# Kernel tuning notes

Hardware: AMD Instinct MI355X
Metric: run time of the kernel (lower is better)

Reference implementation:

```python
import jax, jax.numpy as jnp
import numpy as np

MARGIN = 1.0  # init kwarg 'margin'
N, D = 8192, 128
NUM_CLASSES = 100

def setup_inputs() -> dict:
    key = jax.random.key(0)
    kx, ky = jax.random.split(key)
    x = jax.random.normal(kx, (N, D), dtype=jnp.float32)
    y = jax.random.randint(ky, (N,), 0, NUM_CLASSES, dtype=jnp.int64)
    return {"x": x, "y": y}

def reference(x, y):
    # Squared euclidean pairwise distances: d[i,j] = sum_k (x[i,k] - x[j,k])^2
    # computed via the ||a||^2 + ||b||^2 - 2 a.b expansion to avoid an NxNxD
    # intermediate. Clamp tiny negatives from fp roundoff.
    sq = jnp.sum(x * x, axis=-1)                      # [N]
    d = sq[:, None] + sq[None, :] - 2.0 * (x @ x.T)   # [N, N]
    d = jnp.maximum(d, 0.0)
    same = (y[:, None] == y[None, :]).astype(x.dtype)  # [N, N] positive-pair mask
    # Faithful to the torch module: dissimilar pairs contribute d, similar
    # pairs contribute hinge clamp(margin - d, 0); mean over all N*N pairs.
    loss = jnp.mean((1.0 - same) * d + same * jnp.maximum(MARGIN - d, 0.0))
    return loss
```

## Files before the change

kernel.cpp:

```cpp
#include <hip/hip_runtime.h>


#define N_ROWS 8192
#define DIM    128
#define NCLS   100
#define CAP    224
#define SCB    1024
#define GBPC   8
#define GRAMB  (NCLS * GBPC)
#define NREP   8

typedef _Float16 half8  __attribute__((ext_vector_type(8)));
typedef _Float16 half4v __attribute__((ext_vector_type(4)));
typedef float    float4v __attribute__((ext_vector_type(4)));

__global__ __launch_bounds__(256) void scan_kernel(
    const float* __restrict__ x, const int* __restrict__ y,
    int* __restrict__ cnt, int* __restrict__ idx,
    _Float16* __restrict__ ghrow, float* __restrict__ sqn,
    float* __restrict__ Scol8, float* __restrict__ SQc8)
{
    const int b = blockIdx.x, tid = threadIdx.x;
    const int l = tid & 31, g = tid >> 5;
    const int r = b * 8 + g;
    const int rep = b & (NREP - 1);
    const float4* x4 = (const float4*)x;
    __shared__ float4 colred[256];

    float4 v = x4[r * 32 + l];
    half4v h;
    h[0] = (_Float16)v.x; h[1] = (_Float16)v.y;
    h[2] = (_Float16)v.z; h[3] = (_Float16)v.w;
    *(half4v*)(ghrow + (size_t)r * DIM + l * 4) = h;

    float s = v.x*v.x + v.y*v.y + v.z*v.z + v.w*v.w;
    s += __shfl_xor(s, 1);  s += __shfl_xor(s, 2);  s += __shfl_xor(s, 4);
    s += __shfl_xor(s, 8);  s += __shfl_xor(s, 16);
    const int c = y[r];
    if (l == 0) {
        sqn[r] = s;
        atomicAdd(&SQc8[rep * NCLS + c], s);
        const int p = atomicAdd(&cnt[c], 1);
        if (p < CAP) idx[c * CAP + p] = r;
    }

    colred[tid] = v;
    __syncthreads();
    if (tid < 32) {
        float4 a = colred[tid];
        #pragma unroll
        for (int gg = 1; gg < 8; ++gg) {
            float4 t = colred[tid + 32 * gg];
            a.x += t.x; a.y += t.y; a.z += t.z; a.w += t.w;
        }
        float* dst = Scol8 + rep * DIM;
        atomicAdd(&dst[4 * tid + 0], a.x);
        atomicAdd(&dst[4 * tid + 1], a.y);
        atomicAdd(&dst[4 * tid + 2], a.z);
        atomicAdd(&dst[4 * tid + 3], a.w);
    }
}

__global__ __launch_bounds__(256) void gram_kernel(
    const _Float16* __restrict__ ghrow, const float* __restrict__ sqn,
    const int* __restrict__ idx, const int* __restrict__ cnt,
    const float* __restrict__ Scol8, const float* __restrict__ SQc8,
    float* __restrict__ Hsum, float* __restrict__ SSsum,
    int* __restrict__ done, float* __restrict__ out)
{
    const int c = blockIdx.x >> 3, qq = blockIdx.x & 7, tid = threadIdx.x;
    __shared__ float wred[8];
    __shared__ int   lastFlag;

    const int mtrue = cnt[c];
    const int m = mtrue < CAP ? mtrue : CAP;
    const int ntiles = (m + 15) >> 4;
    const int ntp = ntiles * (ntiles + 1) / 2;

    const int wave = tid >> 6, lane = tid & 63;
    const int lr = lane & 15, q = lane >> 4;
    float hacc = 0.f, dsum = 0.f;
    const int cbase = c * CAP;

    for (int tp = qq * 4 + wave; tp < ntp; tp += 32) {
        int ta = 0, rem = tp;
        while (rem >= ntiles - ta) { rem -= ntiles - ta; ++ta; }
        const int tb = ta + rem;
        const int raI = ta * 16 + lr, rbI = tb * 16 + lr;
        const int rowA = idx[cbase + (raI < m ? raI : m - 1)];
        const int rowB = idx[cbase + (rbI < m ? rbI : m - 1)];
        const half8* ap = (const half8*)(ghrow + (size_t)rowA * DIM + q * 8);
        const half8* bp = (const half8*)(ghrow + (size_t)rowB * DIM + q * 8);
        float4v acc = {0.f, 0.f, 0.f, 0.f};
        #pragma unroll
        for (int kb = 0; kb < 4; ++kb)
            acc = __builtin_amdgcn_mfma_f32_16x16x32_f16(ap[kb * 4], bp[kb * 4], acc, 0, 0, 0);
        const float w = (ta == tb) ? 1.f : 2.f;
        const int bb = rbI;
        const float sqb = (bb < m) ? sqn[rowB] : 0.f;
        const float sqa_own = sqn[rowA];
        #pragma unroll
        for (int i = 0; i < 4; ++i) {
            const int a = ta * 16 + q * 4 + i;
            const float sqa = __shfl(sqa_own, q * 4 + i, 16);
            if (a < m && bb < m) {
                const float dot = acc[i];
                dsum += w * dot;
                if (a != bb) {
                    float d = fmaxf(sqa + sqb - 2.f * dot, 0.f);
                    hacc += w * fmaxf(1.f - d, 0.f);
                }
            }
        }
    }
    #pragma unroll
    for (int off = 32; off > 0; off >>= 1) {
        hacc += __shfl_xor(hacc, off);
        dsum += __shfl_xor(dsum, off);
    }
    if (lane == 0) { wred[wave] = hacc; wred[4 + wave] = dsum; }
    __syncthreads();
    if (tid == 0) {
        float h = wred[0] + wred[1] + wred[2] + wred[3];
        float d = wred[4] + wred[5] + wred[6] + wred[7];
        if (h != 0.f) atomicAdd(Hsum, h);
        if (d != 0.f) atomicAdd(SSsum, d);
        __threadfence();
        int p = atomicAdd(done, 1);
        lastFlag = (p == GRAMB - 1);
    }
    __syncthreads();
    if (!lastFlag) return;

    __threadfence();
    const double Nf = (double)N_ROWS;
    double contrib = 0.0;
    if (tid < DIM) {
        float sc = 0.f;
        #pragma unroll
        for (int k = 0; k < NREP; ++k) sc += Scol8[k * DIM + tid];
        contrib -= 2.0 * (double)sc * (double)sc;
    }
    if (tid < NCLS) {
        float qv = 0.f;
        #pragma unroll
        for (int k = 0; k < NREP; ++k) qv += SQc8[k * NCLS + tid];
        contrib += 2.0 * (double)qv * (Nf - (double)cnt[tid]);
    }
    if (tid == 0) {
        float H  = __hip_atomic_load(Hsum,  __ATOMIC_RELAXED, __HIP_MEMORY_SCOPE_AGENT);
        float SS = __hip_atomic_load(SSsum, __ATOMIC_RELAXED, __HIP_MEMORY_SCOPE_AGENT);
        contrib += 2.0 * (double)SS + (double)H + Nf * 1.0 ;
    }
    __shared__ double dred[256];
    dred[tid] = contrib;
    __syncthreads();
    for (int s = 128; s > 0; s >>= 1) {
        if (tid < s) dred[tid] += dred[tid + s];
        __syncthreads();
    }
    if (tid == 0) out[0] = (float)(dred[0] / (Nf * Nf));
}

extern "C" void kernel_launch(void* const* d_in, const int* in_sizes, int n_in,
                              void* d_out, int out_size, void* d_ws, size_t ws_size,
                              hipStream_t stream) {
    const float* x = (const float*)d_in[0];
    const int*   y = (const int*)d_in[1];

    _Float16* ghrow = (_Float16*)d_ws;
    float* sqn   = (float*)(ghrow + (size_t)N_ROWS * DIM);
    int*   idx   = (int*)(sqn + N_ROWS);
    float* Scol8 = (float*)(idx + NCLS * CAP);
    float* SQc8  = Scol8 + NREP * DIM;
    float* Hsum  = SQc8 + NREP * NCLS;
    float* SSsum = Hsum + 1;
    int*   cnt   = (int*)(SSsum + 1);
    int*   done  = cnt + NCLS;
    const size_t zero_words = NREP * DIM + NREP * NCLS + 2 + NCLS + 1;

    hipMemsetAsync(Scol8, 0, zero_words * sizeof(float), stream);
    scan_kernel<<<SCB,   256, 0, stream>>>(x, y, cnt, idx, ghrow, sqn,
                                           Scol8, SQc8);
    gram_kernel<<<GRAMB, 256, 0, stream>>>(ghrow, sqn, idx, cnt, Scol8, SQc8,
                                           Hsum, SSsum, done, (float*)d_out);
}
```

Measured before the change: 115.1 us.

## Build per-class row lists in-block via ballot scan instead of global atomics

```diff
diff --git a/kernel.cpp b/kernel.cpp
--- a/kernel.cpp
+++ b/kernel.cpp
@@ -15,10 +15,9 @@
 typedef float    float4v __attribute__((ext_vector_type(4)));
 
 __global__ __launch_bounds__(256) void scan_kernel(
-    const float* __restrict__ x, const int* __restrict__ y,
-    int* __restrict__ cnt, int* __restrict__ idx,
+    const float* __restrict__ x,
     _Float16* __restrict__ ghrow, float* __restrict__ sqn,
-    float* __restrict__ Scol8, float* __restrict__ SQc8)
+    float* __restrict__ Scol8)
 {
     const int b = blockIdx.x, tid = threadIdx.x;
     const int l = tid & 31, g = tid >> 5;
@@ -36,13 +35,7 @@
     float s = v.x*v.x + v.y*v.y + v.z*v.z + v.w*v.w;
     s += __shfl_xor(s, 1);  s += __shfl_xor(s, 2);  s += __shfl_xor(s, 4);
     s += __shfl_xor(s, 8);  s += __shfl_xor(s, 16);
-    const int c = y[r];
-    if (l == 0) {
-        sqn[r] = s;
-        atomicAdd(&SQc8[rep * NCLS + c], s);
-        const int p = atomicAdd(&cnt[c], 1);
-        if (p < CAP) idx[c * CAP + p] = r;
-    }
+    if (l == 0) sqn[r] = s;
 
     colred[tid] = v;
     __syncthreads();
@@ -63,32 +56,60 @@
 
 __global__ __launch_bounds__(256) void gram_kernel(
     const _Float16* __restrict__ ghrow, const float* __restrict__ sqn,
-    const int* __restrict__ idx, const int* __restrict__ cnt,
-    const float* __restrict__ Scol8, const float* __restrict__ SQc8,
+    const int* __restrict__ y,
+    const float* __restrict__ Scol8,
     float* __restrict__ Hsum, float* __restrict__ SSsum,
+    double* __restrict__ Dterm,
     int* __restrict__ done, float* __restrict__ out)
 {
     const int c = blockIdx.x >> 3, qq = blockIdx.x & 7, tid = threadIdx.x;
-    __shared__ float wred[8];
+    __shared__ int   lidx[CAP];
+    __shared__ int   lmv[2];
+    __shared__ float wred[12];
     __shared__ int   lastFlag;
 
-    const int mtrue = cnt[c];
-    const int m = mtrue < CAP ? mtrue : CAP;
+    if (tid < 64) {
+        int base = 0;
+        const int4* y4 = (const int4*)y;
+        int4 vv = y4[tid];
+        for (int it = 0; it < N_ROWS / 256; ++it) {
+            const int4 cur = vv;
+            if (it < N_ROWS / 256 - 1) vv = y4[(it + 1) * 64 + tid];
+            const int rbase = (it * 64 + tid) * 4;
+            #pragma unroll
+            for (int j = 0; j < 4; ++j) {
+                const int yi = (j == 0) ? cur.x : (j == 1) ? cur.y
+                             : (j == 2) ? cur.z : cur.w;
+                const unsigned long long mb = __ballot(yi == c);
+                if (yi == c) {
+                    const int pos = base +
+                        (int)__popcll(mb & ((1ull << tid) - 1ull));
+                    if (pos < CAP) lidx[pos] = rbase + j;
+                }
+                base += (int)__popcll(mb);
+            }
+        }
+        if (tid == 0) { lmv[1] = base; lmv[0] = base < CAP ? base : CAP; }
+    }
+    __syncthreads();
+    const int m = lmv[0], mt = lmv[1];
+
     const int ntiles = (m + 15) >> 4;
     const int ntp = ntiles * (ntiles + 1) / 2;
 
     const int wave = tid >> 6, lane = tid & 63;
     const int lr = lane & 15, q = lane >> 4;
     float hacc = 0.f, dsum = 0.f;
-    const int cbase = c * CAP;
+
+    float qv = (qq == 0 && tid < m) ? sqn[lidx[tid]] : 0.f;
 
     for (int tp = qq * 4 + wave; tp < ntp; tp += 32) {
         int ta = 0, rem = tp;
         while (rem >= ntiles - ta) { rem -= ntiles - ta; ++ta; }
         const int tb = ta + rem;
         const int raI = ta * 16 + lr, rbI = tb * 16 + lr;
-        const int rowA = idx[cbase + (raI < m ? raI : m - 1)];
-        const int rowB = idx[cbase + (rbI < m ? rbI : m - 1)];
+        const int rowA = lidx[raI < m ? raI : m - 1];
+        const int rowB = lidx[rbI < m ? rbI : m - 1];
         const half8* ap = (const half8*)(ghrow + (size_t)rowA * DIM + q * 8);
         const half8* bp = (const half8*)(ghrow + (size_t)rowB * DIM + q * 8);
         float4v acc = {0.f, 0.f, 0.f, 0.f};
@@ -117,12 +138,17 @@
     for (int off = 32; off > 0; off >>= 1) {
         hacc += __shfl_xor(hacc, off);
         dsum += __shfl_xor(dsum, off);
-    }
-    if (lane == 0) { wred[wave] = hacc; wred[4 + wave] = dsum; }
+        qv   += __shfl_xor(qv,   off);
+    }
+    if (lane == 0) { wred[wave] = hacc; wred[4 + wave] = dsum; wred[8 + wave] = qv; }
     __syncthreads();
     if (tid == 0) {
         float h = wred[0] + wred[1] + wred[2] + wred[3];
         float d = wred[4] + wred[5] + wred[6] + wred[7];
+        if (qq == 0) {
+            float qs = wred[8] + wred[9] + wred[10] + wred[11];
+            Dterm[c] = 2.0 * (double)qs * ((double)N_ROWS - (double)mt);
+        }
         if (h != 0.f) atomicAdd(Hsum, h);
         if (d != 0.f) atomicAdd(SSsum, d);
         __threadfence();
@@ -141,12 +167,7 @@
         for (int k = 0; k < NREP; ++k) sc += Scol8[k * DIM + tid];
         contrib -= 2.0 * (double)sc * (double)sc;
     }
-    if (tid < NCLS) {
-        float qv = 0.f;
-        #pragma unroll
-        for (int k = 0; k < NREP; ++k) qv += SQc8[k * NCLS + tid];
-        contrib += 2.0 * (double)qv * (Nf - (double)cnt[tid]);
-    }
+    if (tid < NCLS) contrib += Dterm[tid];
     if (tid == 0) {
         float H  = __hip_atomic_load(Hsum,  __ATOMIC_RELAXED, __HIP_MEMORY_SCOPE_AGENT);
         float SS = __hip_atomic_load(SSsum, __ATOMIC_RELAXED, __HIP_MEMORY_SCOPE_AGENT);
@@ -170,18 +191,16 @@
 
     _Float16* ghrow = (_Float16*)d_ws;
     float* sqn   = (float*)(ghrow + (size_t)N_ROWS * DIM);
-    int*   idx   = (int*)(sqn + N_ROWS);
-    float* Scol8 = (float*)(idx + NCLS * CAP);
-    float* SQc8  = Scol8 + NREP * DIM;
-    float* Hsum  = SQc8 + NREP * NCLS;
+    float* Scol8 = sqn + N_ROWS;
+    float* Hsum  = Scol8 + NREP * DIM;
     float* SSsum = Hsum + 1;
-    int*   cnt   = (int*)(SSsum + 1);
-    int*   done  = cnt + NCLS;
-    const size_t zero_words = NREP * DIM + NREP * NCLS + 2 + NCLS + 1;
+    int*   done  = (int*)(SSsum + 1);
+    const size_t zero_words = NREP * DIM + 3;
+    double* Dterm = (double*)(done + 1);
 
     hipMemsetAsync(Scol8, 0, zero_words * sizeof(float), stream);
-    scan_kernel<<<SCB,   256, 0, stream>>>(x, y, cnt, idx, ghrow, sqn,
-                                           Scol8, SQc8);
-    gram_kernel<<<GRAMB, 256, 0, stream>>>(ghrow, sqn, idx, cnt, Scol8, SQc8,
-                                           Hsum, SSsum, done, (float*)d_out);
+    scan_kernel<<<SCB,   256, 0, stream>>>(x, ghrow, sqn, Scol8);
+    gram_kernel<<<GRAMB, 256, 0, stream>>>(ghrow, sqn, y, Scol8,
+                                           Hsum, SSsum, Dterm, done,
+                                           (float*)d_out);
 }
```

Measured after the change: 106.3 us. 7.7% less time.
